# Performance work log

Measured on AMD Instinct MI355X. Metric: run time of the kernel, lower is better.

The kernel has to match this reference:

```python
import jax, jax.numpy as jnp
import numpy as np
import math

# init config (matches init_kwargs); sigma/alpha are squared in __init__
SIGMA2 = 8.0 ** 2
ALPHA2 = 8.0 ** 2
C_SIZE = 512
STRIDE = 8
MINX = 1e-06
M = 100                      # ratio=100 > 1 -> M = int(ratio), capped at 100
K = C_SIZE // STRIDE         # 64 grid cells per axis
G = K * K                    # 4096 density-field cells
B, N = 8, 512                # images, annotated points per image
TWO_PI = 2.0 * math.pi


def setup_inputs():
    key = jax.random.key(0)
    k1, _ = jax.random.split(key)
    points = jax.random.uniform(k1, (B, N, 2), dtype=jnp.float32) * C_SIZE
    st_sizes = jnp.full((B,), float(C_SIZE), dtype=jnp.float32)
    return {"points": points, "st_sizes": st_sizes}


def _per_image(pts, cood):
    # pts: [N,2]; cood: [K]
    x = pts[:, 0]
    y = pts[:, 1]
    dx = x[:, None] - cood[None, :]                 # [N,K]
    dy = y[:, None] - cood[None, :]                 # [N,K]
    # dis_all = y_dis[:, :, None] + x_dis[:, None, :] flattened: g = iy*K + ix
    dis = (dy[:, :, None] ** 2 + dx[:, None, :] ** 2).reshape(pts.shape[0], G)  # [N,G]
    s1 = ALPHA2 + SIGMA2
    s2 = ALPHA2 + SIGMA2 / 2.0
    m = jnp.exp(-0.5 / s1 * dis) / (TWO_PI * s1)    # [N,G]
    tv = jnp.exp(-0.5 / s2 * dis) / (TWO_PI * s2)
    v = (tv / (TWO_PI * 2.0 * SIGMA2)).sum(0) - (m ** 2).sum(0)   # [G] (sel_v == v, no bg)
    # top-M cells by sel_v, then sort indices ascending (ratio>1 branch -> static M)
    inds = jnp.argsort(-v)
    Minds = jnp.sort(inds[:M])                      # [M]
    v = jnp.maximum(v, MINX)                        # add=False -> clamp
    # xf[n, iy*K+ix] = x_n - cood[ix]; yf[n, iy*K+ix] = y_n - cood[iy]
    iy = Minds // K
    ix = Minds % K
    xfM = dx[:, ix]                                 # [N,M]
    yfM = dy[:, iy]                                 # [N,M]
    df = (xfM[:, None, :] - xfM[:, :, None]) ** 2 + (yfM[:, None, :] - yfM[:, :, None]) ** 2
    af = (0.5 * (xfM[:, None, :] + xfM[:, :, None])) ** 2 + (0.5 * (yfM[:, None, :] + yfM[:, :, None])) ** 2
    g1 = jnp.exp(-0.5 / (2.0 * SIGMA2) * df) / (TWO_PI * 2.0 * SIGMA2)          # [N,M,M]
    tmpv2 = (g1 * (jnp.exp(-0.5 / s2 * af) / (TWO_PI * s2))).sum(0) + g1.sum(0)  # [M,M]
    disM = dis[:, Minds]                            # [N,M]
    tmpm2 = jnp.exp(-0.5 / s1 * disM) / (TWO_PI * s1)
    A = tmpv2 - tmpm2.T @ tmpm2                     # [M,M]
    eye = jnp.eye(M, dtype=bool)
    A = jnp.where(eye, 1e-10, A)                    # diag overwritten to 1e-10
    vM = v[Minds] + 1e-10
    tmpA = vM[:, None] * jnp.linalg.inv(A) * vM[None, :] + jnp.diag(vM)
    Bm = jnp.linalg.inv(tmpA)
    return m, v, A, Bm, Minds


def reference(points, st_sizes):
    # st_sizes only matters for use_background=True; kept for signature fidelity
    cood = jnp.arange(0, C_SIZE, STRIDE, dtype=jnp.float32) + STRIDE / 2.0
    m, v, A, Bm, Minds = jax.vmap(lambda p: _per_image(p, cood))(points)
    return m, v, A, Bm, Minds
```

## Files before the change

kernel.cpp:

```cpp
#include <hip/hip_runtime.h>
#include <math.h>

#ifndef M_PI
#define M_PI 3.14159265358979323846
#endif

#define BB 8
#define NN 512
#define KK 64
#define GG 4096
#define MM 100

#define SZ_VD    (BB*GG*8u)
#define OFF_VD   0u
#define SZ_VM    (BB*MM*8u)
#define OFF_VM   (OFF_VD + SZ_VD)
#define SZ_AD    (BB*MM*MM*8u)
#define OFF_AD   (OFF_VM + SZ_VM)
#define OFF_MIND (OFF_AD + SZ_AD)

#define OUT_M  0
#define OUT_V  (BB*NN*GG)
#define OUT_A  (OUT_V + BB*GG)
#define OUT_B  (OUT_A + BB*MM*MM)
#define OUT_MI (OUT_B + BB*MM*MM)

#define MU_VP 4096
#define MU_SE 2048
#define MU_KA 3072
#define MU_IV 7168

__device__ __forceinline__ void m_one_unit(const float* __restrict__ pts,
                                           float* __restrict__ out, int u) {
  int t = u*256 + (int)threadIdx.x;
  int e = t << 2;
  int img = e >> 21;
  int rem = e & ((1 << 21) - 1);
  int n = rem >> 12;
  int g = rem & 4095;
  int iy = g >> 6, ix = g & 63;
  const float CM = (float)(1.0/(2.0*M_PI*128.0));
  float x = pts[(img*NN + n)*2 + 0];
  float y = pts[(img*NN + n)*2 + 1];
  float dy = y - (8.0f*iy + 4.0f);
  float ey = __expf(dy*dy*(-0.5f/128.0f));
  float4 r;
  float dx0 = x - (8.0f*ix + 4.0f);
  float dx1 = x - (8.0f*(ix+1) + 4.0f);
  float dx2 = x - (8.0f*(ix+2) + 4.0f);
  float dx3 = x - (8.0f*(ix+3) + 4.0f);
  r.x = ey*__expf(dx0*dx0*(-0.5f/128.0f))*CM;
  r.y = ey*__expf(dx1*dx1*(-0.5f/128.0f))*CM;
  r.z = ey*__expf(dx2*dx2*(-0.5f/128.0f))*CM;
  r.w = ey*__expf(dx3*dx3*(-0.5f/128.0f))*CM;
  *reinterpret_cast<float4*>(&out[OUT_M + e]) = r;
}

__device__ __forceinline__ float flt_readlane(float v, int l) {
  return __int_as_float(__builtin_amdgcn_readlane(__float_as_int(v), l));
}

__global__ __launch_bounds__(256) void k_vpart(const float* __restrict__ pts,
                                               double* __restrict__ vd,
                                               float* __restrict__ out) {
  __shared__ double sEy2[16][66], sEx2[16][66], sEy3[16][66], sEx3[16][66];
  __shared__ float px[NN], py[NN];
  int bid = blockIdx.x;
  if (bid >= BB*16) { m_one_unit(pts, out, bid - BB*16 + 0); return; }
  int tile = bid & 15;
  int img = bid >> 4;
  int iy0 = (tile >> 2) << 4;
  int ix0 = (tile & 3) << 4;
  int tx = threadIdx.x & 15, ty = threadIdx.x >> 4;
  for (int s = threadIdx.x; s < NN; s += 256) {
    px[s] = pts[(img*NN + s)*2 + 0];
    py[s] = pts[(img*NN + s)*2 + 1];
  }
  double aV = 0.0, aM = 0.0;
  for (int kc = 0; kc < 8; ++kc) {
    int nb = kc << 6;
    __syncthreads();
    for (int s = threadIdx.x; s < 16*64; s += 256) {
      int row = s >> 6, n = s & 63;
      int nn = nb + n;
      double y = (double)py[nn];
      double cy = 8.0*(iy0 + row) + 4.0;
      double dy = y - cy, dy2 = dy*dy;
      sEy2[row][n] = exp(dy2*(-0.5/96.0));
      sEy3[row][n] = exp(dy2*(-1.0/128.0));
      double x = (double)px[nn];
      double cx = 8.0*(ix0 + row) + 4.0;
      double dx = x - cx, dx2 = dx*dx;
      sEx2[row][n] = exp(dx2*(-0.5/96.0));
      sEx3[row][n] = exp(dx2*(-1.0/128.0));
    }
    __syncthreads();
    #pragma unroll 8
    for (int n = 0; n < 64; ++n) {
      aV += sEy2[ty][n]*sEx2[tx][n];
      aM += sEy3[ty][n]*sEx3[tx][n];
    }
  }
  const double CTV = 1.0/((2.0*M_PI*96.0)*(2.0*M_PI*128.0));
  const double CM2 = 1.0/((2.0*M_PI*128.0)*(2.0*M_PI*128.0));
  vd[img*GG + (iy0 + ty)*KK + ix0 + tx] = CTV*aV - CM2*aM;
}

__device__ __forceinline__ void bitonic128(int* a, int tid) {
  for (int kk = 2; kk <= 128; kk <<= 1)
    for (int jj = kk >> 1; jj > 0; jj >>= 1) {
      if (tid < 128) {
        int p = tid ^ jj;
        if (p > tid) {
          int x = a[tid], y = a[p];
          bool up = ((tid & kk) == 0);
          if (up ? (x > y) : (x < y)) { a[tid] = y; a[p] = x; }
        }
      }
      __syncthreads();
    }
}

__global__ __launch_bounds__(256) void k_select(const double* __restrict__ vd,
                                                float* __restrict__ out,
                                                int* __restrict__ minds,
                                                double* __restrict__ vm,
                                                const float* __restrict__ pts) {
  __shared__ unsigned long long ku[GG];
  __shared__ unsigned int hist4[4][256];
  __shared__ unsigned int suf[257];
  __shared__ unsigned long long sPrefPlaced;
  __shared__ unsigned long long sMaskHi;
  __shared__ unsigned int sRem, sPickB, sPickRem, sCGt, sCEq;
  __shared__ int sel[128];
  __shared__ int tie[128];
  int img = blockIdx.x;
  if (img >= BB) { m_one_unit(pts, out, img - BB + MU_VP); return; }
  int tid = threadIdx.x;
  int wv = tid >> 6;
  for (int t = 0; t < 16; ++t) {
    int g = t*256 + tid;
    double v = vd[img*GG + g];
    out[OUT_V + img*GG + g] = (float)fmax(v, 1e-6);
    long long u = __double_as_longlong(v);
    unsigned long long k = (u < 0) ? ~(unsigned long long)u
                                   : ((unsigned long long)u | 0x8000000000000000ull);
    ku[g] = k;
  }
  if (tid == 0) {
    sRem = 100; sPrefPlaced = 0ull; sMaskHi = 0ull;
    sCGt = 0; sCEq = 0; suf[256] = 0;
  }
  for (int shift = 56; shift >= 0; shift -= 8) {
    for (int c = 0; c < 4; ++c) hist4[c][tid] = 0;
    __syncthreads();
    unsigned long long maskHi = sMaskHi, prefP = sPrefPlaced;
    for (int t = 0; t < 16; ++t) {
      int g = t*256 + tid;
      unsigned long long k = ku[g];
      if ((k & maskHi) == prefP) {
        unsigned d = (unsigned)((k >> shift) & 255ull);
        atomicAdd(&hist4[wv][d], 1u);
      }
    }
    __syncthreads();
    suf[tid] = hist4[0][tid] + hist4[1][tid] + hist4[2][tid] + hist4[3][tid];
    __syncthreads();
    for (int off = 1; off < 256; off <<= 1) {
      unsigned add = (tid + off < 256) ? suf[tid + off] : 0u;
      __syncthreads();
      suf[tid] += add;
      __syncthreads();
    }
    unsigned rem = sRem;
    unsigned sgt = (tid < 255) ? suf[tid + 1] : 0u;
    if (suf[tid] >= rem && sgt < rem) { sPickB = (unsigned)tid; sPickRem = rem - sgt; }
    __syncthreads();
    if (tid == 0) {
      sPrefPlaced |= ((unsigned long long)sPickB) << shift;
      sMaskHi     |= (255ull << shift);
      sRem = sPickRem;
    }
    __syncthreads();
  }
  unsigned long long T = sPrefPlaced;
  for (int t = 0; t < 16; ++t) {
    int g = t*256 + tid;
    unsigned long long k = ku[g];
    if (k > T) {
      unsigned p = atomicAdd(&sCGt, 1u);
      sel[p] = g;
    } else if (k == T) {
      unsigned p = atomicAdd(&sCEq, 1u);
      if (p < 128) tie[p] = g;
    }
  }
  __syncthreads();
  unsigned cgt = sCGt, ceq = sCEq, r = sRem;
  if (tid < 128 && tid >= (int)((ceq < 128u) ? ceq : 128u)) tie[tid] = 0x7fffffff;
  __syncthreads();
  bitonic128(tie, tid);
  if (tid < (int)r) sel[cgt + tid] = tie[tid];
  if (tid >= MM && tid < 128) sel[tid] = 0x7fffffff;
  __syncthreads();
  bitonic128(sel, tid);
  if (tid < MM) {
    int mi = sel[tid];
    minds[img*MM + tid] = mi;
    out[OUT_MI + img*MM + tid] = (float)mi;
    vm[img*MM + tid] = fmax(vd[img*GG + mi], 1e-6) + 1e-10;
  }
}

__global__ __launch_bounds__(256) void k_A(const float* __restrict__ pts,
                                           const int* __restrict__ minds,
                                           float* __restrict__ out, double* __restrict__ ad) {
  __shared__ float sxi[16][130], syi[16][130], sti[16][130];
  __shared__ float sxj[16][130], syj[16][130], stj[16][130];
  __shared__ float px[NN], py[NN];
  __shared__ float cxi[16], cyi[16], cxj[16], cyj[16];
  int bid = blockIdx.x;
  if (bid >= BB*28) { m_one_unit(pts, out, bid - BB*28 + MU_VP + MU_SE); return; }
  int img = bid / 28;
  int tile = bid - img*28;
  int it = 0, trem = tile;
  while (trem >= 7 - it) { trem -= 7 - it; ++it; }
  int jt = it + trem;
  int i0 = it*16, j0 = jt*16;
  int tj = threadIdx.x & 15, ti = threadIdx.x >> 4;
  int i = i0 + ti, j = j0 + tj;
  const float CM = (float)(1.0/(2.0*M_PI*128.0));
  const float C1 = (float)(1.0/(2.0*M_PI*128.0));
  const float C2 = (float)(1.0/(2.0*M_PI*96.0));
  for (int s = threadIdx.x; s < NN; s += 256) {
    px[s] = pts[(img*NN + s)*2 + 0];
    py[s] = pts[(img*NN + s)*2 + 1];
  }
  if (threadIdx.x < 16) {
    int gi = i0 + (int)threadIdx.x; if (gi > 99) gi = 99;
    int mi = minds[img*MM + gi];
    cxi[threadIdx.x] = 8.0f*(mi & 63) + 4.0f;
    cyi[threadIdx.x] = 8.0f*(mi >> 6) + 4.0f;
  } else if (threadIdx.x < 32) {
    int r = (int)threadIdx.x - 16;
    int gj = j0 + r; if (gj > 99) gj = 99;
    int mj = minds[img*MM + gj];
    cxj[r] = 8.0f*(mj & 63) + 4.0f;
    cyj[r] = 8.0f*(mj >> 6) + 4.0f;
  }
  float aV = 0.0f, aM = 0.0f;
  for (int nc = 0; nc < NN; nc += 128) {
    __syncthreads();
    for (int s = threadIdx.x; s < 16*128; s += 256) {
      int row = s >> 7, n = s & 127;
      float x = px[nc + n], y = py[nc + n];
      float fxi = x - cxi[row], fyi = y - cyi[row];
      sxi[row][n] = fxi; syi[row][n] = fyi;
      sti[row][n] = __expf((fxi*fxi + fyi*fyi)*(-0.5f/128.0f))*CM;
      float fxj = x - cxj[row], fyj = y - cyj[row];
      sxj[row][n] = fxj; syj[row][n] = fyj;
      stj[row][n] = __expf((fxj*fxj + fyj*fyj)*(-0.5f/128.0f))*CM;
    }
    __syncthreads();
    #pragma unroll 4
    for (int n = 0; n < 128; ++n) {
      float xi = sxi[ti][n], yi = syi[ti][n], tii = sti[ti][n];
      float xj = sxj[tj][n], yj = syj[tj][n], tjj = stj[tj][n];
      float ddx = xj - xi, ddy = yj - yi;
      float df = ddx*ddx + ddy*ddy;
      float sx = 0.5f*(xi + xj), sy = 0.5f*(yi + yj);
      float af = sx*sx + sy*sy;
      float g1 = __expf(df*(-0.5f/128.0f))*C1;
      float h  = __expf(af*(-0.5f/96.0f))*C2;
      aV += g1 + g1*h;
      aM += tii*tjj;
    }
  }
  if (i < 100 && j < 100) {
    double val = (i == j) ? 1e-10 : ((double)aV - (double)aM);
    out[OUT_A + (img*MM + i)*MM + j] = (float)val;
    ad[(img*MM + i)*MM + j] = val;
    if (it != jt) {
      out[OUT_A + (img*MM + j)*MM + i] = (float)val;
      ad[(img*MM + j)*MM + i] = val;
    }
  }
}

__global__ __launch_bounds__(256)
void k_inv_m(const double* __restrict__ ad,
             const double* __restrict__ vm,
             const float* __restrict__ pts,
             float* __restrict__ out) {
  __shared__ float S[128*17];
  __shared__ float Pr[16*113];
  __shared__ float svm[112];
  if (blockIdx.x >= BB) {
    m_one_unit(pts, out, (int)blockIdx.x - BB + MU_VP + MU_SE + MU_KA);
    return;
  }
  int img = blockIdx.x;
  int tx = threadIdx.x & 15, ty = threadIdx.x >> 4;
  float C[7][7];
  if (threadIdx.x < 100) svm[threadIdx.x] = (float)vm[img*MM + threadIdx.x];
  #pragma unroll
  for (int a = 0; a < 7; ++a) {
    int r = ty + 16*a;
    #pragma unroll
    for (int b = 0; b < 7; ++b) {
      int j = tx + 16*b;
      float v2 = (r < 100 && j < 100) ? (float)ad[(img*MM + r)*MM + j] : 0.0f;
      if (r == j && r < 100) v2 += (float)vm[img*MM + r];
      C[a][b] = v2;
    }
  }
  for (int p = 0; p < 7; ++p) {
    int k0 = p*16;
    int nbp = (p == 6) ? 4 : 16;
    #pragma unroll
    for (int a = 0; a < 7; ++a) {
      int r = ty + 16*a;
      float val = 0.0f;
      #pragma unroll
      for (int b = 0; b < 7; ++b) if (b == p) val = C[a][b];
      S[r*17 + tx] = (r < 100 && tx < nbp) ? val : 0.0f;
    }
    {
      float pv[7];
      #pragma unroll
      for (int b = 0; b < 7; ++b) pv[b] = 0.0f;
      #pragma unroll
      for (int a = 0; a < 7; ++a) {
        #pragma unroll
        for (int b = 0; b < 7; ++b) if (a == p) pv[b] = C[a][b];
      }
      #pragma unroll
      for (int b = 0; b < 7; ++b) Pr[ty*113 + tx + 16*b] = pv[b];
    }
    __syncthreads();
    if (threadIdx.x < 64) {
      int lane = threadIdx.x;
      float P0[16], P1[16];
      #pragma unroll
      for (int c = 0; c < 16; ++c) {
        P0[c] = S[lane*17 + c];
        P1[c] = (lane + 64 < 112) ? S[(lane + 64)*17 + c] : 0.0f;
      }
      #pragma unroll
      for (int kk = 0; kk < 16; ++kk) {
        if (kk < nbp) {
          int kg = k0 + kk;
          int r1 = lane + 64;
          bool khigh = kg >= 64; int kl = kg & 63;
          float pivinv = 1.0f / flt_readlane(khigh ? P1[kk] : P0[kk], kl);
          float pr[16];
          #pragma unroll
          for (int c = 0; c < 16; ++c) {
            float pv = flt_readlane(khigh ? P1[c] : P0[c], kl);
            pr[c] = (c == kk) ? pivinv : pv*pivinv;
          }
          {
            float f = P0[kk];
            if (lane == kg) {
              #pragma unroll
              for (int c = 0; c < 16; ++c) P0[c] = pr[c];
            } else {
              #pragma unroll
              for (int c = 0; c < 16; ++c) P0[c] = ((c == kk) ? 0.0f : P0[c]) - f*pr[c];
            }
          }
          {
            float f = P1[kk];
            if (r1 == kg) {
              #pragma unroll
              for (int c = 0; c < 16; ++c) P1[c] = pr[c];
            } else {
              #pragma unroll
              for (int c = 0; c < 16; ++c) P1[c] = ((c == kk) ? 0.0f : P1[c]) - f*pr[c];
            }
          }
        }
      }
      #pragma unroll
      for (int c = 0; c < 16; ++c) {
        S[lane*17 + c] = P0[c];
        if (lane + 64 < 112) S[(lane + 64)*17 + c] = P1[c];
      }
    }
    __syncthreads();
    #pragma unroll
    for (int a = 0; a < 7; ++a) {
      int r = ty + 16*a;
      bool prow_ = (r >= k0) && (r < k0 + 16);
      #pragma unroll
      for (int b = 0; b < 7; ++b) {
        if (r >= 100 || b == p || prow_) C[a][b] = 0.0f;
      }
    }
    #pragma unroll 4
    for (int t = 0; t < 16; ++t) {
      bool tok = (t < nbp);
      float bt[7], sa[7];
      #pragma unroll
      for (int b = 0; b < 7; ++b) bt[b] = tok ? Pr[t*113 + tx + 16*b] : 0.0f;
      #pragma unroll
      for (int a = 0; a < 7; ++a) sa[a] = S[(ty + 16*a)*17 + t];
      #pragma unroll
      for (int a = 0; a < 7; ++a)
        #pragma unroll
        for (int b = 0; b < 7; ++b) C[a][b] += sa[a]*bt[b];
    }
    #pragma unroll
    for (int a = 0; a < 7; ++a) {
      int r = ty + 16*a;
      float sval = S[r*17 + tx];
      #pragma unroll
      for (int b = 0; b < 7; ++b) if (b == p) C[a][b] = sval;
    }
    __syncthreads();
  }
  #pragma unroll
  for (int a = 0; a < 7; ++a) {
    int r = ty + 16*a; if (r >= 100) continue;
    float dinv = 1.0f / svm[r];
    #pragma unroll
    for (int b = 0; b < 7; ++b) {
      int c = tx + 16*b; if (c >= 100) continue;
      float val = ((c == r) ? dinv : 0.0f) - C[a][b];
      out[OUT_B + (img*MM + r)*MM + c] = val;
    }
  }
}

extern "C" void kernel_launch(void* const* d_in, const int* in_sizes, int n_in,
                              void* d_out, int out_size, void* d_ws, size_t ws_size,
                              hipStream_t stream) {
  const float* pts = (const float*)d_in[0];
  float* out = (float*)d_out;
  char* ws = (char*)d_ws;
  double* vd  = (double*)(ws + OFF_VD);
  double* vmd = (double*)(ws + OFF_VM);
  double* ad  = (double*)(ws + OFF_AD);
  int* minds = (int*)(ws + OFF_MIND);

  hipLaunchKernelGGL(k_vpart, dim3(BB*16 + MU_VP), dim3(256), 0, stream, pts, vd, out);
  hipLaunchKernelGGL(k_select, dim3(BB + MU_SE), dim3(256), 0, stream, vd, out, minds, vmd, pts);
  hipLaunchKernelGGL(k_A, dim3(BB*28 + MU_KA), dim3(256), 0, stream, pts, minds, out, ad);
  hipLaunchKernelGGL(k_inv_m, dim3(BB + MU_IV), dim3(256), 0, stream, ad, vmd, pts, out);
}
```

Before: 230.6 us.

## Fuse top-M selection into A-matrix kernel, recomputing selection per tile block

Merges the selection kernel and the A-matrix kernel into one launch. Every A tile block redoes the radix top-100 selection for its image in a shared-memory union, and only tile 0 writes v, Minds and vM. This drops one kernel launch and its inter-kernel barrier, and no longer passes minds through global memory. In exchange the selection work is repeated 28 times per image, which lengthens each A block's critical path. The m-field filler work is redistributed among the remaining kernels.

```diff
diff --git a/kernel.cpp b/kernel.cpp
--- a/kernel.cpp
+++ b/kernel.cpp
@@ -26,9 +26,8 @@
 #define OUT_MI (OUT_B + BB*MM*MM)
 
 #define MU_VP 4096
-#define MU_SE 2048
-#define MU_KA 3072
-#define MU_IV 7168
+#define MU_AS 2048
+#define MU_IV 10240
 
 __device__ __forceinline__ void m_one_unit(const float* __restrict__ pts,
                                            float* __restrict__ out, int u) {
@@ -106,6 +105,23 @@
   vd[img*GG + (iy0 + ty)*KK + ix0 + tx] = CTV*aV - CM2*aM;
 }
 
+union AselU {
+  struct {
+    unsigned long long ku[GG];
+    unsigned int hist4[4][256];
+    unsigned int suf[257];
+    unsigned long long sPrefPlaced, sMaskHi;
+    unsigned int sRem, sPickB, sPickRem, sCGt, sCEq;
+    int tie[128];
+  } se;
+  struct {
+    float sxi[16][130], syi[16][130], sti[16][130];
+    float sxj[16][130], syj[16][130], stj[16][130];
+    float px[NN], py[NN];
+    float cxi[16], cyi[16], cxj[16], cyj[16];
+  } ka;
+};
+
 __device__ __forceinline__ void bitonic128(int* a, int tid) {
   for (int kk = 2; kk <= 128; kk <<= 1)
     for (int jj = kk >> 1; jj > 0; jj >>= 1) {
@@ -121,151 +137,138 @@
     }
 }
 
-__global__ __launch_bounds__(256) void k_select(const double* __restrict__ vd,
-                                                float* __restrict__ out,
-                                                int* __restrict__ minds,
-                                                double* __restrict__ vm,
-                                                const float* __restrict__ pts) {
-  __shared__ unsigned long long ku[GG];
-  __shared__ unsigned int hist4[4][256];
-  __shared__ unsigned int suf[257];
-  __shared__ unsigned long long sPrefPlaced;
-  __shared__ unsigned long long sMaskHi;
-  __shared__ unsigned int sRem, sPickB, sPickRem, sCGt, sCEq;
-  __shared__ int sel[128];
-  __shared__ int tie[128];
-  int img = blockIdx.x;
-  if (img >= BB) { m_one_unit(pts, out, img - BB + MU_VP); return; }
+__global__ __launch_bounds__(256) void k_Asel(const float* __restrict__ pts,
+                                              const double* __restrict__ vd,
+                                              float* __restrict__ out,
+                                              double* __restrict__ ad,
+                                              double* __restrict__ vm) {
+  __shared__ AselU u;
+  __shared__ int selFinal[128];
+  int bid = blockIdx.x;
+  if (bid >= BB*28) { m_one_unit(pts, out, bid - BB*28 + MU_VP); return; }
+  int img = bid / 28;
+  int tile = bid - img*28;
+  bool tile0 = (tile == 0);
   int tid = threadIdx.x;
   int wv = tid >> 6;
+
   for (int t = 0; t < 16; ++t) {
     int g = t*256 + tid;
     double v = vd[img*GG + g];
-    out[OUT_V + img*GG + g] = (float)fmax(v, 1e-6);
-    long long u = __double_as_longlong(v);
-    unsigned long long k = (u < 0) ? ~(unsigned long long)u
-                                   : ((unsigned long long)u | 0x8000000000000000ull);
-    ku[g] = k;
+    if (tile0) out[OUT_V + img*GG + g] = (float)fmax(v, 1e-6);
+    long long w = __double_as_longlong(v);
+    unsigned long long k = (w < 0) ? ~(unsigned long long)w
+                                   : ((unsigned long long)w | 0x8000000000000000ull);
+    u.se.ku[g] = k;
   }
   if (tid == 0) {
-    sRem = 100; sPrefPlaced = 0ull; sMaskHi = 0ull;
-    sCGt = 0; sCEq = 0; suf[256] = 0;
+    u.se.sRem = 100; u.se.sPrefPlaced = 0ull; u.se.sMaskHi = 0ull;
+    u.se.sCGt = 0; u.se.sCEq = 0; u.se.suf[256] = 0;
   }
   for (int shift = 56; shift >= 0; shift -= 8) {
-    for (int c = 0; c < 4; ++c) hist4[c][tid] = 0;
-    __syncthreads();
-    unsigned long long maskHi = sMaskHi, prefP = sPrefPlaced;
+    for (int c = 0; c < 4; ++c) u.se.hist4[c][tid] = 0;
+    __syncthreads();
+    unsigned long long maskHi = u.se.sMaskHi, prefP = u.se.sPrefPlaced;
     for (int t = 0; t < 16; ++t) {
       int g = t*256 + tid;
-      unsigned long long k = ku[g];
+      unsigned long long k = u.se.ku[g];
       if ((k & maskHi) == prefP) {
         unsigned d = (unsigned)((k >> shift) & 255ull);
-        atomicAdd(&hist4[wv][d], 1u);
-      }
-    }
-    __syncthreads();
-    suf[tid] = hist4[0][tid] + hist4[1][tid] + hist4[2][tid] + hist4[3][tid];
+        atomicAdd(&u.se.hist4[wv][d], 1u);
+      }
+    }
+    __syncthreads();
+    u.se.suf[tid] = u.se.hist4[0][tid] + u.se.hist4[1][tid]
+                  + u.se.hist4[2][tid] + u.se.hist4[3][tid];
     __syncthreads();
     for (int off = 1; off < 256; off <<= 1) {
-      unsigned add = (tid + off < 256) ? suf[tid + off] : 0u;
+      unsigned add = (tid + off < 256) ? u.se.suf[tid + off] : 0u;
       __syncthreads();
-      suf[tid] += add;
+      u.se.suf[tid] += add;
       __syncthreads();
     }
-    unsigned rem = sRem;
-    unsigned sgt = (tid < 255) ? suf[tid + 1] : 0u;
-    if (suf[tid] >= rem && sgt < rem) { sPickB = (unsigned)tid; sPickRem = rem - sgt; }
+    unsigned rem = u.se.sRem;
+    unsigned sgt = (tid < 255) ? u.se.suf[tid + 1] : 0u;
+    if (u.se.suf[tid] >= rem && sgt < rem) { u.se.sPickB = (unsigned)tid; u.se.sPickRem = rem - sgt; }
     __syncthreads();
     if (tid == 0) {
-      sPrefPlaced |= ((unsigned long long)sPickB) << shift;
-      sMaskHi     |= (255ull << shift);
-      sRem = sPickRem;
-    }
-    __syncthreads();
-  }
-  unsigned long long T = sPrefPlaced;
+      u.se.sPrefPlaced |= ((unsigned long long)u.se.sPickB) << shift;
+      u.se.sMaskHi     |= (255ull << shift);
+      u.se.sRem = u.se.sPickRem;
+    }
+    __syncthreads();
+  }
+  unsigned long long T = u.se.sPrefPlaced;
   for (int t = 0; t < 16; ++t) {
     int g = t*256 + tid;
-    unsigned long long k = ku[g];
+    unsigned long long k = u.se.ku[g];
     if (k > T) {
-      unsigned p = atomicAdd(&sCGt, 1u);
-      sel[p] = g;
+      unsigned p = atomicAdd(&u.se.sCGt, 1u);
+      selFinal[p] = g;
     } else if (k == T) {
-      unsigned p = atomicAdd(&sCEq, 1u);
-      if (p < 128) tie[p] = g;
+      unsigned p = atomicAdd(&u.se.sCEq, 1u);
+      if (p < 128) u.se.tie[p] = g;
     }
   }
   __syncthreads();
-  unsigned cgt = sCGt, ceq = sCEq, r = sRem;
-  if (tid < 128 && tid >= (int)((ceq < 128u) ? ceq : 128u)) tie[tid] = 0x7fffffff;
+  unsigned cgt = u.se.sCGt, ceq = u.se.sCEq, r = u.se.sRem;
+  if (tid < 128 && tid >= (int)((ceq < 128u) ? ceq : 128u)) u.se.tie[tid] = 0x7fffffff;
   __syncthreads();
-  bitonic128(tie, tid);
-  if (tid < (int)r) sel[cgt + tid] = tie[tid];
-  if (tid >= MM && tid < 128) sel[tid] = 0x7fffffff;
+  bitonic128(u.se.tie, tid);
+  if (tid < (int)r) selFinal[cgt + tid] = u.se.tie[tid];
+  if (tid >= MM && tid < 128) selFinal[tid] = 0x7fffffff;
   __syncthreads();
-  bitonic128(sel, tid);
-  if (tid < MM) {
-    int mi = sel[tid];
-    minds[img*MM + tid] = mi;
+  bitonic128(selFinal, tid);
+  if (tile0 && tid < MM) {
+    int mi = selFinal[tid];
     out[OUT_MI + img*MM + tid] = (float)mi;
     vm[img*MM + tid] = fmax(vd[img*GG + mi], 1e-6) + 1e-10;
   }
-}
-
-__global__ __launch_bounds__(256) void k_A(const float* __restrict__ pts,
-                                           const int* __restrict__ minds,
-                                           float* __restrict__ out, double* __restrict__ ad) {
-  __shared__ float sxi[16][130], syi[16][130], sti[16][130];
-  __shared__ float sxj[16][130], syj[16][130], stj[16][130];
-  __shared__ float px[NN], py[NN];
-  __shared__ float cxi[16], cyi[16], cxj[16], cyj[16];
-  int bid = blockIdx.x;
-  if (bid >= BB*28) { m_one_unit(pts, out, bid - BB*28 + MU_VP + MU_SE); return; }
-  int img = bid / 28;
-  int tile = bid - img*28;
+  __syncthreads();
+
   int it = 0, trem = tile;
   while (trem >= 7 - it) { trem -= 7 - it; ++it; }
   int jt = it + trem;
   int i0 = it*16, j0 = jt*16;
-  int tj = threadIdx.x & 15, ti = threadIdx.x >> 4;
+  int tj = tid & 15, ti = tid >> 4;
   int i = i0 + ti, j = j0 + tj;
   const float CM = (float)(1.0/(2.0*M_PI*128.0));
   const float C1 = (float)(1.0/(2.0*M_PI*128.0));
   const float C2 = (float)(1.0/(2.0*M_PI*96.0));
-  for (int s = threadIdx.x; s < NN; s += 256) {
-    px[s] = pts[(img*NN + s)*2 + 0];
-    py[s] = pts[(img*NN + s)*2 + 1];
-  }
-  if (threadIdx.x < 16) {
-    int gi = i0 + (int)threadIdx.x; if (gi > 99) gi = 99;
-    int mi = minds[img*MM + gi];
-    cxi[threadIdx.x] = 8.0f*(mi & 63) + 4.0f;
-    cyi[threadIdx.x] = 8.0f*(mi >> 6) + 4.0f;
-  } else if (threadIdx.x < 32) {
-    int r = (int)threadIdx.x - 16;
-    int gj = j0 + r; if (gj > 99) gj = 99;
-    int mj = minds[img*MM + gj];
-    cxj[r] = 8.0f*(mj & 63) + 4.0f;
-    cyj[r] = 8.0f*(mj >> 6) + 4.0f;
+  for (int s = tid; s < NN; s += 256) {
+    u.ka.px[s] = pts[(img*NN + s)*2 + 0];
+    u.ka.py[s] = pts[(img*NN + s)*2 + 1];
+  }
+  if (tid < 16) {
+    int gi = i0 + tid; if (gi > 99) gi = 99;
+    int mi = selFinal[gi];
+    u.ka.cxi[tid] = 8.0f*(mi & 63) + 4.0f;
+    u.ka.cyi[tid] = 8.0f*(mi >> 6) + 4.0f;
+  } else if (tid < 32) {
+    int rr = tid - 16;
+    int gj = j0 + rr; if (gj > 99) gj = 99;
+    int mj = selFinal[gj];
+    u.ka.cxj[rr] = 8.0f*(mj & 63) + 4.0f;
+    u.ka.cyj[rr] = 8.0f*(mj >> 6) + 4.0f;
   }
   float aV = 0.0f, aM = 0.0f;
   for (int nc = 0; nc < NN; nc += 128) {
     __syncthreads();
-    for (int s = threadIdx.x; s < 16*128; s += 256) {
+    for (int s = tid; s < 16*128; s += 256) {
       int row = s >> 7, n = s & 127;
-      float x = px[nc + n], y = py[nc + n];
-      float fxi = x - cxi[row], fyi = y - cyi[row];
-      sxi[row][n] = fxi; syi[row][n] = fyi;
-      sti[row][n] = __expf((fxi*fxi + fyi*fyi)*(-0.5f/128.0f))*CM;
-      float fxj = x - cxj[row], fyj = y - cyj[row];
-      sxj[row][n] = fxj; syj[row][n] = fyj;
-      stj[row][n] = __expf((fxj*fxj + fyj*fyj)*(-0.5f/128.0f))*CM;
+      float x = u.ka.px[nc + n], y = u.ka.py[nc + n];
+      float fxi = x - u.ka.cxi[row], fyi = y - u.ka.cyi[row];
+      u.ka.sxi[row][n] = fxi; u.ka.syi[row][n] = fyi;
+      u.ka.sti[row][n] = __expf((fxi*fxi + fyi*fyi)*(-0.5f/128.0f))*CM;
+      float fxj = x - u.ka.cxj[row], fyj = y - u.ka.cyj[row];
+      u.ka.sxj[row][n] = fxj; u.ka.syj[row][n] = fyj;
+      u.ka.stj[row][n] = __expf((fxj*fxj + fyj*fyj)*(-0.5f/128.0f))*CM;
     }
     __syncthreads();
     #pragma unroll 4
     for (int n = 0; n < 128; ++n) {
-      float xi = sxi[ti][n], yi = syi[ti][n], tii = sti[ti][n];
-      float xj = sxj[tj][n], yj = syj[tj][n], tjj = stj[tj][n];
+      float xi = u.ka.sxi[ti][n], yi = u.ka.syi[ti][n], tii = u.ka.sti[ti][n];
+      float xj = u.ka.sxj[tj][n], yj = u.ka.syj[tj][n], tjj = u.ka.stj[tj][n];
       float ddx = xj - xi, ddy = yj - yi;
       float df = ddx*ddx + ddy*ddy;
       float sx = 0.5f*(xi + xj), sy = 0.5f*(yi + yj);
@@ -296,7 +299,7 @@
   __shared__ float Pr[16*113];
   __shared__ float svm[112];
   if (blockIdx.x >= BB) {
-    m_one_unit(pts, out, (int)blockIdx.x - BB + MU_VP + MU_SE + MU_KA);
+    m_one_unit(pts, out, (int)blockIdx.x - BB + MU_VP + MU_AS);
     return;
   }
   int img = blockIdx.x;
@@ -441,10 +444,8 @@
   double* vd  = (double*)(ws + OFF_VD);
   double* vmd = (double*)(ws + OFF_VM);
   double* ad  = (double*)(ws + OFF_AD);
-  int* minds = (int*)(ws + OFF_MIND);
 
   hipLaunchKernelGGL(k_vpart, dim3(BB*16 + MU_VP), dim3(256), 0, stream, pts, vd, out);
-  hipLaunchKernelGGL(k_select, dim3(BB + MU_SE), dim3(256), 0, stream, vd, out, minds, vmd, pts);
-  hipLaunchKernelGGL(k_A, dim3(BB*28 + MU_KA), dim3(256), 0, stream, pts, minds, out, ad);
+  hipLaunchKernelGGL(k_Asel, dim3(BB*28 + MU_AS), dim3(256), 0, stream, pts, vd, out, ad, vmd);
   hipLaunchKernelGGL(k_inv_m, dim3(BB + MU_IV), dim3(256), 0, stream, ad, vmd, pts, out);
 }
```

Result: no change. 230.9 us (+0.1%).
